# Performance work log

Hardware: AMD Instinct MI355X
Metric: run time of the kernel (lower is better)

## Reference

```python
import jax, jax.numpy as jnp
import numpy as np

B, N, DE, H, DH = 2, 1024, 1024, 16, 64
DK = H * DH  # total complex qkv dim per stream
MIN_EXP = -30.0
EPS = 1e-4


def setup_inputs():
    key = jax.random.key(0)
    ks = jax.random.split(key, 8)

    def g(i, shape, sc=1.0):
        return jax.random.normal(ks[i], shape, jnp.float32) * sc

    # RoPE-style per-head frequencies for the conjugate-paired half-dims
    freqs = 10000.0 ** (-np.arange(DH // 2, dtype=np.float64) / (DH // 2))
    omega = jnp.asarray(np.tile(freqs[None, :], (H, 1)), jnp.float32)
    return {
        "x": g(0, (B, N, DE)),
        "Wq": g(1, (DE, 2 * DK), 1.0 / np.sqrt(DE)),
        "Wk": g(2, (DE, 2 * DK), 1.0 / np.sqrt(DE)),
        "Wv": g(3, (DE, 2 * DK), 1.0 / np.sqrt(DE)),
        "Wo": g(4, (2 * DK, DE), 1.0 / np.sqrt(2 * DK)),
        "omega": omega,
        "mu_raw": g(5, (H,)) - 2.0,          # pre-sigmoid decay rates
        "sigma_raw": g(6, (H,)),              # pre-softplus process noise
        "eta_raw": jnp.ones((H,), jnp.float32),
        "gamma_raw": jnp.ones((H,), jnp.float32),
        "tau": jnp.ones((H,), jnp.float32),   # inverse temperature
        "nu_raw": jnp.ones((H,), jnp.float32) * 4.0,  # robustness dof
    }


def reference(x, Wq, Wk, Wv, Wo, omega, mu_raw, sigma_raw, eta_raw, gamma_raw, tau, nu_raw):
    B_, N_, _ = x.shape
    H_, d_half = omega.shape
    DH_ = 2 * d_half
    DKt = H_ * DH_

    def cproj(W):
        z = x @ W                          # [B,N,2D] real/imag packed
        D = W.shape[1] // 2
        zc = jax.lax.complex(z[..., :D], z[..., D:])
        return zc.reshape(B_, N_, H_, DH_)

    q, k, v = cproj(Wq), cproj(Wk), cproj(Wv)

    # complex-conjugate-constrained rotations: omega stacked as [w, -w]
    om = jnp.concatenate([omega, -omega], axis=-1)              # [H,DH]
    t = jnp.arange(N_, dtype=jnp.float32)
    ang = t[:, None, None] * om[None]                           # [N,H,DH]
    phase = jax.lax.complex(jnp.cos(ang), jnp.sin(ang))
    qr = q * phase[None]
    kr = k * phase[None]

    # isotropic SDE decay kernel  E_rel = exp(-mu * |t_i - t_j|)
    mu = jax.nn.sigmoid(mu_raw) + EPS                           # [H]
    dt = jnp.abs(t[:, None] - t[None, :])                       # [N,N]
    E = jnp.exp(jnp.clip(-mu[:, None, None] * dt[None], MIN_EXP, 0.0))  # [H,N,N]

    # Re<q_i, Phi(dt) k_j>  (rotation carried by phases, decay by E)
    s = jnp.einsum('bihd,bjhd->bhij', qr, jnp.conj(kr)).real    # [B,H,N,N]
    qn = (q.real ** 2 + q.imag ** 2).sum(-1).transpose(0, 2, 1)  # [B,H,N]
    kn = (k.real ** 2 + k.imag ** 2).sum(-1).transpose(0, 2, 1)

    # Lyapunov-propagated uncertainty: P(dt) = sigma^2/(2mu)(1 - E^2) + eta^2 + gamma^2
    sigma_sq = jax.nn.softplus(sigma_raw)
    eta_sq = jax.nn.softplus(eta_raw)
    gamma_sq = jax.nn.softplus(gamma_raw)
    V = (sigma_sq / (2.0 * mu))[:, None, None] * (1.0 - E * E) \
        + (eta_sq + gamma_sq)[:, None, None]                    # [H,N,N]

    # per-head Mahalanobis residual under the SDE forecast
    maha = jnp.maximum(qn[..., None] + (E * E)[None] * kn[:, :, None, :]
                       - 2.0 * E[None] * s, 0.0) / V[None]      # [B,H,N,N]

    # robust nu-thresholding (Student-t style) + Gaussian normalization term
    nu = jax.nn.softplus(nu_raw)
    coef = (-0.5 * tau * (nu + DH_))[None, :, None, None]
    logits = coef * jnp.log1p(maha / nu[None, :, None, None]) \
             - 0.5 * DH_ * jnp.log(V)[None]

    causal = (t[:, None] >= t[None, :])
    logits = jnp.where(causal[None, None], logits, -jnp.inf)
    A = jax.nn.softmax(logits, axis=-1)                         # [B,H,N,N]

    out = jnp.einsum('bhij,bjhd->bihd', A.astype(v.dtype), v)   # complex [B,N,H,DH]
    y = jnp.concatenate([out.real.reshape(B_, N_, DKt),
                         out.imag.reshape(B_, N_, DKt)], axis=-1)
    return y @ Wo                                               # [B,N,DE]
```

## Files before the change

kernel.cpp:

```cpp
#include <hip/hip_runtime.h>
#include <math.h>

#define BB      2
#define NN      1024
#define DE_     1024
#define HH      16
#define TWO_DK  2048
#define PK      4194304
#define TBLR    1092

typedef float f32x4  __attribute__((ext_vector_type(4)));
typedef short bf16x8 __attribute__((ext_vector_type(8)));

__device__ __forceinline__ short f2bf(float f) {
    unsigned u = __float_as_uint(f);
    unsigned r = (u + 0x7fffu + ((u >> 16) & 1u)) >> 16;
    return (short)r;
}
__device__ __forceinline__ float bf2f(short v) {
    return __uint_as_float(((unsigned)(unsigned short)v) << 16);
}

__device__ __forceinline__ float fexp2(float x) { return __builtin_amdgcn_exp2f(x); }
__device__ __forceinline__ float flog2(float x) { return __builtin_amdgcn_logf(x); }

#define GLDS16(g, l) __builtin_amdgcn_global_load_lds(                        \
    (const __attribute__((address_space(1))) unsigned int*)(g),               \
    (__attribute__((address_space(3))) unsigned int*)(l), 16, 0, 0)
#define GLDS4(g, l) __builtin_amdgcn_global_load_lds(                         \
    (const __attribute__((address_space(1))) unsigned int*)(g),               \
    (__attribute__((address_space(3))) unsigned int*)(l), 4, 0, 0)

__constant__ int jIT[24] = {7,14,15,15, 6,12,13,13,14, 5,10,11,11,12,
                            4, 8, 9, 9,10, 3, 8, 2, 1, 0};
__constant__ int jJ0[24] = {0, 0, 0, 8, 0, 0, 0, 7, 8, 0, 0, 0, 6, 7,
                            0, 0, 0, 5, 6, 0, 5, 0, 0, 0};
__constant__ int jJ1[24] = {7, 7, 7,15, 6, 6, 6,13,14, 5, 5, 5,11,12,
                            4, 4, 4, 9,10, 3, 8, 2, 1, 0};
__constant__ int jPS[24] = {0, 1, 1, 2, 0, 1, 1, 2, 2, 0, 1, 1, 2, 2,
                            0, 1, 1, 2, 2, 0, 2, 0, 0, 0};

__global__ __launch_bounds__(256) void prep(
    const float* __restrict__ x,
    const float* __restrict__ Wq, const float* __restrict__ Wk,
    const float* __restrict__ Wv, const float* __restrict__ Wo,
    const float* __restrict__ mu_raw, const float* __restrict__ sigma_raw,
    const float* __restrict__ eta_raw, const float* __restrict__ gamma_raw,
    short* __restrict__ xb, short* __restrict__ wt, short* __restrict__ wot,
    float4* __restrict__ tbl) {
    const int z = blockIdx.z;
    if (z == 4) {
        const int flat = blockIdx.y * 32 + blockIdx.x;
        const int i = (flat * 256 + threadIdx.x) * 8;
        float4 v0 = *(const float4*)&x[i];
        float4 v1 = *(const float4*)&x[i + 4];
        short4 o0, o1;
        o0.x = f2bf(v0.x); o0.y = f2bf(v0.y); o0.z = f2bf(v0.z); o0.w = f2bf(v0.w);
        o1.x = f2bf(v1.x); o1.y = f2bf(v1.y); o1.z = f2bf(v1.z); o1.w = f2bf(v1.w);
        *(short4*)&xb[i] = o0; *(short4*)&xb[i + 4] = o1;
        return;
    }
    if (z == 3 && blockIdx.x >= 16) {
        const int idx = blockIdx.y * 16 + (blockIdx.x - 16);
        if (idx >= 80) return;
        const int h = idx / 5, rb = idx % 5;
        const int r = rb * 256 + threadIdx.x;
        if (r >= TBLR) return;
        const float mu = 1.f / (1.f + expf(-mu_raw[h])) + 1e-4f;
        const float Ac = log1pf(expf(sigma_raw[h])) / (2.f * mu);
        const float Cc = log1pf(expf(eta_raw[h])) + log1pf(expf(gamma_raw[h]));
        const float arg = fminf(fmaxf(-mu * (float)(r - 64), -30.f), 0.f);
        const float E   = expf(arg);
        const float V   = fmaf(Ac, 1.f - E * E, Cc);
        tbl[h * TBLR + r] = make_float4(2.f * E, 1.f / V, -32.f * log2f(V), E * E);
        return;
    }
    const float* in; short* out; int R, C;
    if (z < 3) { if (blockIdx.y >= 16) return;
                 in = (z == 0) ? Wq : (z == 1) ? Wk : Wv;
                 out = wt + (size_t)z * 2097152; R = 1024; C = 2048; }
    else       { in = Wo; out = wot; R = 2048; C = 1024; }
    __shared__ float t[64][65];
    const int c0 = blockIdx.x * 64, r0 = blockIdx.y * 64;
    const int tr = threadIdx.x >> 4, tc4 = (threadIdx.x & 15) * 4;
#pragma unroll
    for (int s = 0; s < 4; ++s) {
        const int r = tr + s * 16;
        float4 v = *(const float4*)&in[(size_t)(r0 + r) * C + c0 + tc4];
        t[r][tc4] = v.x; t[r][tc4 + 1] = v.y; t[r][tc4 + 2] = v.z; t[r][tc4 + 3] = v.w;
    }
    __syncthreads();
#pragma unroll
    for (int s = 0; s < 4; ++s) {
        const int oc = tr + s * 16;
        short4 o;
        o.x = f2bf(t[tc4 + 0][oc]); o.y = f2bf(t[tc4 + 1][oc]);
        o.z = f2bf(t[tc4 + 2][oc]); o.w = f2bf(t[tc4 + 3][oc]);
        *(short4*)&out[(size_t)(c0 + oc) * R + r0 + tc4] = o;
    }
}

__global__ __launch_bounds__(256) void gemm_qkv_rot2(
    const short* __restrict__ A, const short* __restrict__ wt,
    const float* __restrict__ omega,
    short* __restrict__ qb, short* __restrict__ kb, short* __restrict__ vtb,
    float* __restrict__ qn_, float* __restrict__ kn_) {
    __shared__ __align__(16) short As[128 * 64];
    __shared__ __align__(16) short Bs[128 * 64];
    __shared__ float sN[2][128];
    const int tid = threadIdx.x;
    const int m0  = blockIdx.x * 128;
    const int h   = blockIdx.y;
    const short* W = wt + (size_t)blockIdx.z * 2097152;

    const short* aP[4]; const short* bP[4]; int ldsoff[4];
#pragma unroll
    for (int i = 0; i < 4; ++i) {
        const int c   = i * 256 + tid;
        const int row = c >> 3;
        const int src = ((c & 7) ^ (row & 7)) << 3;
        ldsoff[i] = c * 8;
        aP[i] = A + (size_t)(m0 + row) * 1024 + src;
        const int t_ = row >> 5, u_ = (row >> 4) & 1, dcol = t_ * 16 + (row & 15);
        bP[i] = W + (size_t)(u_ * 1024 + h * 64 + dcol) * 1024 + src;
    }

    const int lane = tid & 63, w = tid >> 6;
    const int wr = (w >> 1) * 64, hsel = w & 1, wc = hsel * 64;
    const int fr = lane & 15;
    const int fo = (lane >> 4) << 3;
    const int sw = (fr & 7) << 3;

    f32x4 acc[4][4];
#pragma unroll
    for (int a = 0; a < 4; ++a)
#pragma unroll
        for (int b = 0; b < 4; ++b) acc[a][b] = (f32x4){0.f, 0.f, 0.f, 0.f};

    for (int k0 = 0; k0 < 1024; k0 += 64) {
#pragma unroll
        for (int i = 0; i < 4; ++i) GLDS16(aP[i] + k0, &As[ldsoff[i]]);
#pragma unroll
        for (int i = 0; i < 4; ++i) GLDS16(bP[i] + k0, &Bs[ldsoff[i]]);
        __syncthreads();
#pragma unroll
        for (int ks = 0; ks < 64; ks += 32) {
            bf16x8 af[4], bf[4];
#pragma unroll
            for (int a = 0; a < 4; ++a)
                af[a] = *(const bf16x8*)&As[(wr + a * 16 + fr) * 64 + ((ks + fo) ^ sw)];
#pragma unroll
            for (int b = 0; b < 4; ++b)
                bf[b] = *(const bf16x8*)&Bs[(wc + b * 16 + fr) * 64 + ((ks + fo) ^ sw)];
#pragma unroll
            for (int a = 0; a < 4; ++a)
#pragma unroll
                for (int b = 0; b < 4; ++b)
                    acc[a][b] = __builtin_amdgcn_mfma_f32_16x16x32_bf16(
                        af[a], bf[b], acc[a][b], 0, 0, 0);
        }
        __syncthreads();
    }

    const int cq = (lane >> 4) * 4, l15 = lane & 15;
    const int bh  = (m0 >> 10) * 16 + h;
    const int nb0 = (m0 & 1023) + wr + cq;

    if (blockIdx.z == 2) {
#pragma unroll
        for (int a = 0; a < 4; ++a) {
#pragma unroll
            for (int b = 0; b < 4; ++b) {
                const int cl = wc + b * 16;
                const int dd = ((cl >> 4) & 1) * 64 + (cl >> 5) * 16 + l15;
                short4 o;
                o.x = f2bf(acc[a][b][0]); o.y = f2bf(acc[a][b][1]);
                o.z = f2bf(acc[a][b][2]); o.w = f2bf(acc[a][b][3]);
                *(short4*)&vtb[((size_t)bh * 128 + dd) * 1024 + nb0 + a * 16] = o;
            }
        }
        return;
    }
    float* nout = (blockIdx.z == 0) ? qn_ : kn_;
    short* obuf = (blockIdx.z == 0) ? qb  : kb;

#pragma unroll
    for (int a = 0; a < 4; ++a) {
        float ns[4] = {0.f, 0.f, 0.f, 0.f};
#pragma unroll
        for (int b = 0; b < 4; ++b)
#pragma unroll
            for (int r = 0; r < 4; ++r)
                ns[r] = fmaf(acc[a][b][r], acc[a][b][r], ns[r]);
#pragma unroll
        for (int m2 = 1; m2 < 16; m2 <<= 1)
#pragma unroll
            for (int r = 0; r < 4; ++r) ns[r] += __shfl_xor(ns[r], m2);
        if (l15 == 0)
#pragma unroll
            for (int r = 0; r < 4; ++r) sN[hsel][wr + a * 16 + cq + r] = ns[r];
    }
    __syncthreads();
    if (tid < 128)
        nout[(size_t)bh * 1024 + (m0 & 1023) + tid] = sN[0][tid] + sN[1][tid];

#pragma unroll
    for (int p = 0; p < 2; ++p) {
        const int d = (hsel * 2 + p) * 16 + l15;
        const float om = (d < 32) ? omega[h * 32 + d] : -omega[h * 32 + d - 32];
#pragma unroll
        for (int a = 0; a < 4; ++a) {
#pragma unroll
            for (int r = 0; r < 4; ++r) {
                const int n2 = nb0 + a * 16 + r;
                float sn, cs;
                __sincosf((float)n2 * om, &sn, &cs);
                const float re = acc[a][2 * p][r], im = acc[a][2 * p + 1][r];
                short* orow = obuf + ((size_t)bh * 1024 + n2) * 128;
                orow[d]      = f2bf(re * cs - im * sn);
                orow[64 + d] = f2bf(re * sn + im * cs);
            }
        }
    }
}

__global__ __launch_bounds__(256) void attn_mfma(
    const short* __restrict__ qr, const short* __restrict__ kr,
    const short* __restrict__ vt,
    const float* __restrict__ qn, const float* __restrict__ kn,
    const float4* __restrict__ tbl,
    const float* __restrict__ tau_p, const float* __restrict__ nu_raw,
    short* __restrict__ y, short* __restrict__ po0, float* __restrict__ pml) {
    __shared__ __align__(16) short Ks[2][64 * 128];
    __shared__ __align__(16) short Vs[2][128 * 64];
    __shared__ __align__(16) short Ps[64 * 72];
    __shared__ __align__(16) float4 sT[2][128];
    __shared__ float sKn[2][64];

    const int bx   = blockIdx.x;
    const int xcd  = bx & 7;
    const int rest = bx >> 3;
    const int jrk  = rest >> 2;
    const int bh   = xcd * 4 + (rest & 3);
    const int h    = bh & 15;
    const int it   = jIT[jrk];
    const int j0j  = jJ0[jrk];
    const int j1j  = jJ1[jrk];
    const int psel = jPS[jrk];
    const int i0   = it * 64;
    const int pq   = bh * 8 + (it - 8);

    const int tid  = threadIdx.x;
    const int lane = tid & 63, w = tid >> 6;
    const int quad = lane >> 4, l15 = lane & 15;

    const float nu     = log1pf(expf(nu_raw[h]));
    const float coef   = -0.5f * tau_p[h] * (nu + 64.0f);
    const float inv_nu = 1.f / nu;

    const short* Qb  = qr + (size_t)bh * NN * 128;
    const short* Kb  = kr + (size_t)bh * NN * 128;
    const short* Vtb = vt + (size_t)bh * 128 * NN;

#define STAGE(JT, P) do {                                                     \
        const int j0_ = (JT) * 64, dt0_ = i0 - j0_;                           \
        _Pragma("unroll")                                                     \
        for (int i_ = 0; i_ < 4; ++i_) {                                      \
            const int c_ = i_ * 256 + tid, row_ = c_ >> 4;                    \
            const int src_ = ((c_ & 15) ^ (row_ & 7)) * 8;                    \
            GLDS16(Kb + (size_t)(j0_ + row_) * 128 + src_, &Ks[P][c_ * 8]);   \
        }                                                                     \
        _Pragma("unroll")                                                     \
        for (int i_ = 0; i_ < 4; ++i_) {                                      \
            const int c_ = i_ * 256 + tid, d_ = c_ >> 3;                      \
            const int src_ = ((c_ & 7) ^ (d_ & 7)) * 8;                       \
            GLDS16(Vtb + (size_t)d_ * NN + j0_ + src_, &Vs[P][c_ * 8]);       \
        }                                                                     \
        if (w == 0) {                                                         \
            GLDS16(tbl + h * TBLR + 1 + dt0_ + lane, &sT[P][lane]);           \
            GLDS16(tbl + h * TBLR + 65 + dt0_ + lane, &sT[P][64 + lane]);     \
        } else if (w == 1) {                                                  \
            GLDS4(kn + (size_t)bh * NN + j0_ + lane, &sKn[P][lane]);          \
        }                                                                     \
    } while (0)

    bf16x8 qf[4];
    const int arow = i0 + w * 16 + l15;
#pragma unroll
    for (int ks = 0; ks < 4; ++ks)
        qf[ks] = *(const bf16x8*)&Qb[(size_t)arow * 128 + ks * 32 + quad * 8];

    float mrow[4];
    f32x4 o[8];
    f32x4 o9 = (f32x4){0.f, 0.f, 0.f, 0.f};
#pragma unroll
    for (int r = 0; r < 4; ++r) mrow[r] = -INFINITY;
#pragma unroll
    for (int s = 0; s < 8; ++s) o[s] = (f32x4){0.f, 0.f, 0.f, 0.f};
    float qn4[4];
#pragma unroll
    for (int r = 0; r < 4; ++r)
        qn4[r] = qn[(size_t)bh * NN + i0 + w * 16 + quad * 4 + r];

    const bf16x8 onesv = (bf16x8){0x3F80, 0x3F80, 0x3F80, 0x3F80,
                                  0x3F80, 0x3F80, 0x3F80, 0x3F80};

    STAGE(j0j, 0);
    __syncthreads();

    for (int jt = j0j; jt <= j1j; ++jt) {
        const int p = (jt - j0j) & 1;
        if (jt < j1j) STAGE(jt + 1, 1 - p);

        f32x4 sAcc[4];
#pragma unroll
        for (int s = 0; s < 4; ++s) sAcc[s] = (f32x4){0.f, 0.f, 0.f, 0.f};
#pragma unroll
        for (int ks = 0; ks < 4; ++ks) {
#pragma unroll
            for (int s = 0; s < 4; ++s) {
                const int brow = s * 16 + l15;
                bf16x8 bK = *(const bf16x8*)&Ks[p][brow * 128 +
                                                  (((ks * 4 + quad) ^ (brow & 7)) * 8)];
                sAcc[s] = __builtin_amdgcn_mfma_f32_16x16x32_bf16(qf[ks], bK, sAcc[s], 0, 0, 0);
            }
        }

        float al[4];
        bool anyr = false;
#pragma unroll
        for (int r = 0; r < 4; ++r) {
            const int row = w * 16 + quad * 4 + r;
            float lg[4];
#pragma unroll
            for (int s = 0; s < 4; ++s) {
                const int col = s * 16 + l15;
                const float4 T = sT[p][row - col + 63];
                const float sv = sAcc[s][r];
                const float t1 = fmaf(T.w, sKn[p][col], qn4[r]);
                const float maha = fmaxf(fmaf(-T.x, sv, t1), 0.f) * T.y;
                float v = fmaf(coef, flog2(fmaf(maha, inv_nu, 1.f)), T.z);
                if (jt == it && col > row) v = -INFINITY;
                lg[s] = v;
            }
            float mx = fmaxf(fmaxf(lg[0], lg[1]), fmaxf(lg[2], lg[3]));
            mx = fmaxf(mx, __shfl_xor(mx, 1));
            mx = fmaxf(mx, __shfl_xor(mx, 2));
            mx = fmaxf(mx, __shfl_xor(mx, 4));
            mx = fmaxf(mx, __shfl_xor(mx, 8));
            const bool resc = mx > mrow[r] + 16.f;
            const float mu_ = resc ? mx : mrow[r];
            al[r] = resc ? fexp2(mrow[r] - mx) : 1.f;
            mrow[r] = mu_;
            anyr = anyr || resc;
#pragma unroll
            for (int s = 0; s < 4; ++s) {
                const float pv = fexp2(lg[s] - mu_);
                Ps[row * 72 + s * 16 + l15] = f2bf(pv);
            }
        }
        if (anyr) {
#pragma unroll
            for (int s = 0; s < 8; ++s)
#pragma unroll
                for (int r = 0; r < 4; ++r) o[s][r] *= al[r];
#pragma unroll
            for (int r = 0; r < 4; ++r) o9[r] *= al[r];
        }

#pragma unroll
        for (int jc = 0; jc < 2; ++jc) {
            bf16x8 aP = *(const bf16x8*)&Ps[(w * 16 + l15) * 72 + jc * 32 + quad * 8];
#pragma unroll
            for (int sub = 0; sub < 8; ++sub) {
                const int d = sub * 16 + l15;
                bf16x8 bV = *(const bf16x8*)&Vs[p][d * 64 + (((jc * 4 + quad) ^ (d & 7)) * 8)];
                o[sub] = __builtin_amdgcn_mfma_f32_16x16x32_bf16(aP, bV, o[sub], 0, 0, 0);
            }
            o9 = __builtin_amdgcn_mfma_f32_16x16x32_bf16(aP, onesv, o9, 0, 0, 0);
        }
        if (jt < j1j) __syncthreads();
    }
#undef STAGE

    short* dst = (psel == 1) ? po0 : y;
    const size_t rbase = (psel == 1) ? (size_t)pq * 64 : ((size_t)bh * NN + i0);
#pragma unroll
    for (int r = 0; r < 4; ++r) {
        const int lrow = w * 16 + quad * 4 + r;
        const float inv = 1.f / o9[r];
        const size_t base = (rbase + lrow) * 128;
#pragma unroll
        for (int sub = 0; sub < 8; ++sub)
            dst[base + sub * 16 + l15] = f2bf(o[sub][r] * inv);
        if (psel != 0 && l15 == 0)
            pml[(pq * 2 + (psel - 1)) * 64 + lrow] = mrow[r] + flog2(o9[r]);
    }
}

__global__ __launch_bounds__(256) void attn_merge(
    const short* __restrict__ po0, const float* __restrict__ pml,
    short* __restrict__ y) {
    const int qs = blockIdx.x;
    const int bh = qs >> 3, it = (qs & 7) + 8;
    const int t = threadIdx.x;
    const int row = t >> 2, dc = (t & 3) * 32;
    const float m1 = pml[(qs * 2 + 0) * 64 + row];
    const float m2 = pml[(qs * 2 + 1) * 64 + row];
    const float mx = fmaxf(m1, m2);
    const float w1 = fexp2(m1 - mx), w2 = fexp2(m2 - mx);
    const float inv = 1.f / (w1 + w2);
    const float a = w1 * inv, b = w2 * inv;
    const short* s1 = po0 + ((size_t)qs * 64 + row) * 128 + dc;
    short*       s2 = y + ((size_t)bh * NN + it * 64 + row) * 128 + dc;
#pragma unroll
    for (int i = 0; i < 32; i += 8) {
        bf16x8 v1 = *(const bf16x8*)(s1 + i);
        bf16x8 v2 = *(const bf16x8*)(s2 + i);
        bf16x8 ov;
#pragma unroll
        for (int k = 0; k < 8; ++k)
            ov[k] = f2bf(a * bf2f(v1[k]) + b * bf2f(v2[k]));
        *(bf16x8*)(s2 + i) = ov;
    }
}

__global__ __launch_bounds__(256) void gemm_out64(
    const short* __restrict__ yb, const short* __restrict__ wot,
    float* __restrict__ out) {
    __shared__ __align__(16) short As[64 * 64];
    __shared__ __align__(16) short Bs[64 * 64];
    const int tid = threadIdx.x;
    const int m0  = blockIdx.x * 64;
    const int n0  = blockIdx.y * 64;
    const int bb  = m0 >> 10;

    int aPre[2], aOff[2]; const short* bP[2];
#pragma unroll
    for (int i = 0; i < 2; ++i) {
        const int c = i * 256 + tid, row = c >> 3;
        const int src = ((c & 7) ^ (row & 7)) << 3;
        aPre[i] = ((m0 & 1023) + row) * 128 + src;
        bP[i] = wot + (size_t)(n0 + row) * 2048 + src;
        aOff[i] = c * 8;
    }

    const int lane = tid & 63, w = tid >> 6;
    const int wr = (w >> 1) * 32, wc = (w & 1) * 32;
    const int fr = lane & 15;
    const int fo = (lane >> 4) << 3;
    const int sw = (fr & 7) << 3;

    f32x4 acc[2][2];
#pragma unroll
    for (int a = 0; a < 2; ++a)
#pragma unroll
        for (int b = 0; b < 2; ++b) acc[a][b] = (f32x4){0.f, 0.f, 0.f, 0.f};

    for (int k0 = 0; k0 < 2048; k0 += 64) {
        const int hh = (k0 >> 6) & 15, im = k0 >> 10;
        const short* ab = yb + ((size_t)(bb * 16 + hh) << 17) + im * 64;
#pragma unroll
        for (int i = 0; i < 2; ++i) GLDS16(ab + aPre[i], &As[aOff[i]]);
#pragma unroll
        for (int i = 0; i < 2; ++i) GLDS16(bP[i] + k0, &Bs[aOff[i]]);
        __syncthreads();
#pragma unroll
        for (int ks = 0; ks < 64; ks += 32) {
            bf16x8 af[2], bf[2];
#pragma unroll
            for (int a = 0; a < 2; ++a)
                af[a] = *(const bf16x8*)&As[(wr + a * 16 + fr) * 64 + ((ks + fo) ^ sw)];
#pragma unroll
            for (int b = 0; b < 2; ++b)
                bf[b] = *(const bf16x8*)&Bs[(wc + b * 16 + fr) * 64 + ((ks + fo) ^ sw)];
#pragma unroll
            for (int a = 0; a < 2; ++a)
#pragma unroll
                for (int b = 0; b < 2; ++b)
                    acc[a][b] = __builtin_amdgcn_mfma_f32_16x16x32_bf16(
                        af[a], bf[b], acc[a][b], 0, 0, 0);
        }
        __syncthreads();
    }

    const int cq = (lane >> 4) * 4, l15 = lane & 15;
#pragma unroll
    for (int a = 0; a < 2; ++a)
#pragma unroll
        for (int b = 0; b < 2; ++b)
#pragma unroll
            for (int r = 0; r < 4; ++r)
                out[(size_t)(m0 + wr + a * 16 + cq + r) * 1024 +
                    (n0 + wc + b * 16 + l15)] = acc[a][b][r];
}

extern "C" void kernel_launch(void* const* d_in, const int* in_sizes, int n_in,
                              void* d_out, int out_size, void* d_ws, size_t ws_size,
                              hipStream_t stream) {
    const float* x         = (const float*)d_in[0];
    const float* Wq        = (const float*)d_in[1];
    const float* Wk        = (const float*)d_in[2];
    const float* Wv        = (const float*)d_in[3];
    const float* Wo        = (const float*)d_in[4];
    const float* omega     = (const float*)d_in[5];
    const float* mu_raw    = (const float*)d_in[6];
    const float* sigma_raw = (const float*)d_in[7];
    const float* eta_raw   = (const float*)d_in[8];
    const float* gamma_raw = (const float*)d_in[9];
    const float* tau       = (const float*)d_in[10];
    const float* nu_raw    = (const float*)d_in[11];
    float* out = (float*)d_out;

    short*  qb  = (short*)d_ws;
    short*  kb  = qb + PK;
    short*  vtb = kb + PK;
    float*  qn  = (float*)(vtb + PK);
    float*  kn  = qn + 32768;
    float4* tbl = (float4*)(kn + 32768);
    short*  wot = (short*)(tbl + HH * TBLR);
    short*  wt  = wot + 2097152;
    short*  xb  = wt + 3 * 2097152;
    short*  yb  = wt;
    short*  po0 = wt + 4194304;
    float*  pml = (float*)xb;

    prep<<<dim3(32, 32, 5), 256, 0, stream>>>(
        x, Wq, Wk, Wv, Wo, mu_raw, sigma_raw, eta_raw, gamma_raw,
        xb, wt, wot, tbl);
    gemm_qkv_rot2<<<dim3(16, 16, 3), 256, 0, stream>>>(
        xb, wt, omega, qb, kb, vtb, qn, kn);
    attn_mfma<<<dim3(768), 256, 0, stream>>>(
        qb, kb, vtb, qn, kn, tbl, tau, nu_raw, yb, po0, pml);
    attn_merge<<<dim3(256), 256, 0, stream>>>(po0, pml, yb);
    gemm_out64<<<dim3(32, 16), 256, 0, stream>>>(yb, wot, out);
}
```

Baseline: 201.4 us.

## Double-buffer LDS tiles in QKV and output projection GEMMs

Both the fused QKV/rotation GEMM and the output projection GEMM now keep two shared-memory stages for their A and B tiles. The async global-to-LDS load for tile k+1 is issued before the MFMA work on tile k, and the trailing barrier is skipped on the last iteration. The aim is to hide global load latency behind matrix-core compute instead of stalling at a barrier on every K step. In exchange, shared memory per block doubles (to 64KB in the QKV GEMM), which may lower the number of resident blocks per CU.

```diff
diff --git a/kernel.cpp b/kernel.cpp
--- a/kernel.cpp
+++ b/kernel.cpp
@@ -105,8 +105,8 @@
     const float* __restrict__ omega,
     short* __restrict__ qb, short* __restrict__ kb, short* __restrict__ vtb,
     float* __restrict__ qn_, float* __restrict__ kn_) {
-    __shared__ __align__(16) short As[128 * 64];
-    __shared__ __align__(16) short Bs[128 * 64];
+    __shared__ __align__(16) short As[2][128 * 64];
+    __shared__ __align__(16) short Bs[2][128 * 64];
     __shared__ float sN[2][128];
     const int tid = threadIdx.x;
     const int m0  = blockIdx.x * 128;
@@ -137,21 +137,30 @@
 #pragma unroll
         for (int b = 0; b < 4; ++b) acc[a][b] = (f32x4){0.f, 0.f, 0.f, 0.f};
 
-    for (int k0 = 0; k0 < 1024; k0 += 64) {
-#pragma unroll
-        for (int i = 0; i < 4; ++i) GLDS16(aP[i] + k0, &As[ldsoff[i]]);
-#pragma unroll
-        for (int i = 0; i < 4; ++i) GLDS16(bP[i] + k0, &Bs[ldsoff[i]]);
-        __syncthreads();
+#pragma unroll
+    for (int i = 0; i < 4; ++i) GLDS16(aP[i], &As[0][ldsoff[i]]);
+#pragma unroll
+    for (int i = 0; i < 4; ++i) GLDS16(bP[i], &Bs[0][ldsoff[i]]);
+    __syncthreads();
+
+    for (int kt = 0; kt < 16; ++kt) {
+        const int p = kt & 1;
+        if (kt < 15) {
+            const int k1 = (kt + 1) * 64;
+#pragma unroll
+            for (int i = 0; i < 4; ++i) GLDS16(aP[i] + k1, &As[1 - p][ldsoff[i]]);
+#pragma unroll
+            for (int i = 0; i < 4; ++i) GLDS16(bP[i] + k1, &Bs[1 - p][ldsoff[i]]);
+        }
 #pragma unroll
         for (int ks = 0; ks < 64; ks += 32) {
             bf16x8 af[4], bf[4];
 #pragma unroll
             for (int a = 0; a < 4; ++a)
-                af[a] = *(const bf16x8*)&As[(wr + a * 16 + fr) * 64 + ((ks + fo) ^ sw)];
+                af[a] = *(const bf16x8*)&As[p][(wr + a * 16 + fr) * 64 + ((ks + fo) ^ sw)];
 #pragma unroll
             for (int b = 0; b < 4; ++b)
-                bf[b] = *(const bf16x8*)&Bs[(wc + b * 16 + fr) * 64 + ((ks + fo) ^ sw)];
+                bf[b] = *(const bf16x8*)&Bs[p][(wc + b * 16 + fr) * 64 + ((ks + fo) ^ sw)];
 #pragma unroll
             for (int a = 0; a < 4; ++a)
 #pragma unroll
@@ -159,7 +168,7 @@
                     acc[a][b] = __builtin_amdgcn_mfma_f32_16x16x32_bf16(
                         af[a], bf[b], acc[a][b], 0, 0, 0);
         }
-        __syncthreads();
+        if (kt < 15) __syncthreads();
     }
 
     const int cq = (lane >> 4) * 4, l15 = lane & 15;
@@ -428,8 +437,8 @@
 __global__ __launch_bounds__(256) void gemm_out64(
     const short* __restrict__ yb, const short* __restrict__ wot,
     float* __restrict__ out) {
-    __shared__ __align__(16) short As[64 * 64];
-    __shared__ __align__(16) short Bs[64 * 64];
+    __shared__ __align__(16) short As[2][64 * 64];
+    __shared__ __align__(16) short Bs[2][64 * 64];
     const int tid = threadIdx.x;
     const int m0  = blockIdx.x * 64;
     const int n0  = blockIdx.y * 64;
@@ -457,23 +466,31 @@
 #pragma unroll
         for (int b = 0; b < 2; ++b) acc[a][b] = (f32x4){0.f, 0.f, 0.f, 0.f};
 
-    for (int k0 = 0; k0 < 2048; k0 += 64) {
-        const int hh = (k0 >> 6) & 15, im = k0 >> 10;
-        const short* ab = yb + ((size_t)(bb * 16 + hh) << 17) + im * 64;
-#pragma unroll
-        for (int i = 0; i < 2; ++i) GLDS16(ab + aPre[i], &As[aOff[i]]);
-#pragma unroll
-        for (int i = 0; i < 2; ++i) GLDS16(bP[i] + k0, &Bs[aOff[i]]);
-        __syncthreads();
+#define OSTAGE(KT, P) do {                                                    \
+        const int k0_ = (KT) * 64;                                            \
+        const int hh_ = (k0_ >> 6) & 15, im_ = k0_ >> 10;                     \
+        const short* ab_ = yb + ((size_t)(bb * 16 + hh_) << 17) + im_ * 64;   \
+        _Pragma("unroll")                                                     \
+        for (int i_ = 0; i_ < 2; ++i_) GLDS16(ab_ + aPre[i_], &As[P][aOff[i_]]); \
+        _Pragma("unroll")                                                     \
+        for (int i_ = 0; i_ < 2; ++i_) GLDS16(bP[i_] + k0_, &Bs[P][aOff[i_]]);   \
+    } while (0)
+
+    OSTAGE(0, 0);
+    __syncthreads();
+
+    for (int kt = 0; kt < 32; ++kt) {
+        const int p = kt & 1;
+        if (kt < 31) OSTAGE(kt + 1, 1 - p);
 #pragma unroll
         for (int ks = 0; ks < 64; ks += 32) {
             bf16x8 af[2], bf[2];
 #pragma unroll
             for (int a = 0; a < 2; ++a)
-                af[a] = *(const bf16x8*)&As[(wr + a * 16 + fr) * 64 + ((ks + fo) ^ sw)];
+                af[a] = *(const bf16x8*)&As[p][(wr + a * 16 + fr) * 64 + ((ks + fo) ^ sw)];
 #pragma unroll
             for (int b = 0; b < 2; ++b)
-                bf[b] = *(const bf16x8*)&Bs[(wc + b * 16 + fr) * 64 + ((ks + fo) ^ sw)];
+                bf[b] = *(const bf16x8*)&Bs[p][(wc + b * 16 + fr) * 64 + ((ks + fo) ^ sw)];
 #pragma unroll
             for (int a = 0; a < 2; ++a)
 #pragma unroll
@@ -481,8 +498,9 @@
                     acc[a][b] = __builtin_amdgcn_mfma_f32_16x16x32_bf16(
                         af[a], bf[b], acc[a][b], 0, 0, 0);
         }
-        __syncthreads();
-    }
+        if (kt < 31) __syncthreads();
+    }
+#undef OSTAGE
 
     const int cq = (lane >> 4) * 4, l15 = lane & 15;
 #pragma unroll
```

Result: slower. 212.5 us (+5.5%).
